# Kernel tuning notes

Measured on AMD Instinct MI355X. Metric: run time of the kernel, lower is better.

## Reference

```python
import jax, jax.numpy as jnp
import numpy as np

DEPTH_REF = jnp.array([28.01, 16.32], dtype=jnp.float32)
DIM_REF = jnp.array([[3.88, 1.63, 1.53], [0.84, 1.76, 0.66], [1.78, 1.52, 1.78]], dtype=jnp.float32)
TOPK = 50
DET_THRESHOLD = 0.25
PI = 3.14159265358979


def nms_hm(heat, kernel=3):
    # 3x3 max-pool NMS: keep peaks, zero everything else
    pad = (kernel - 1) // 2
    hmax = jax.lax.reduce_window(heat, -jnp.inf, jax.lax.max,
                                 (1, 1, kernel, kernel), (1, 1, 1, 1),
                                 [(0, 0), (0, 0), (pad, pad), (pad, pad)])
    return jnp.where(hmax == heat, heat, 0.0)


def select_topk(heat, K):
    B, C, H, W = heat.shape
    scores_all, inds_all = jax.lax.top_k(heat.reshape(B, C, H * W), K)  # [B,C,K]
    ys_all = (inds_all // W).astype(jnp.float32)
    xs_all = (inds_all % W).astype(jnp.float32)
    scores, inds = jax.lax.top_k(scores_all.reshape(B, C * K), K)       # [B,K] over classes
    clses = (inds // K).astype(jnp.float32)
    topk_inds = jnp.take_along_axis(inds_all.reshape(B, C * K), inds, axis=1)
    ys = jnp.take_along_axis(ys_all.reshape(B, C * K), inds, axis=1)
    xs = jnp.take_along_axis(xs_all.reshape(B, C * K), inds, axis=1)
    return scores, topk_inds, clses, ys, xs


def select_point_of_interest(index, feature_maps):
    B, Cf, H, W = feature_maps.shape
    fm = feature_maps.transpose(0, 2, 3, 1).reshape(B, H * W, Cf)
    return jnp.take_along_axis(fm, index[:, :, None], axis=1)  # [B,K,Cf]


def encode_box3d(rotys, dims, locs):
    # dims = (l, h, w); corner signs reproduce SMOKE's gather pattern
    N = rotys.shape[0]
    c, s = jnp.cos(rotys), jnp.sin(rotys)
    z, o = jnp.zeros_like(c), jnp.ones_like(c)
    ry = jnp.stack([c, z, s, z, o, z, -s, z, c], axis=1).reshape(N, 3, 3)
    sx = jnp.array([-0.5, 0.5, 0.5, 0.5, 0.5, -0.5, -0.5, -0.5], dtype=dims.dtype)
    sy = jnp.array([-1., -1., 0., 0., -1., -1., 0., 0.], dtype=dims.dtype)
    sz = jnp.array([-0.5, -0.5, -0.5, 0.5, 0.5, 0.5, 0.5, -0.5], dtype=dims.dtype)
    corners = jnp.stack([dims[:, 0:1] * sx, dims[:, 1:2] * sy, dims[:, 2:3] * sz], axis=1)  # [N,3,8]
    return jnp.einsum('nij,njk->nik', ry, corners) + locs[:, :, None]


def setup_inputs() -> dict:
    key = jax.random.key(0)
    k1, k2 = jax.random.split(key)
    B, C, H, W = 32, 3, 192, 640
    IMG_W, IMG_H = 4 * W, 4 * H
    pred_heatmap = jax.random.uniform(k1, (B, C, H, W), dtype=jnp.float32)
    pred_regression = jax.random.normal(k2, (B, 8, H, W), dtype=jnp.float32) * 0.5
    # affine image->heatmap (scale 1/4), invertible
    tm = jnp.array([[0.25, 0., 0.], [0., 0.25, 0.], [0., 0., 1.]], dtype=jnp.float32)
    trans_mat = jnp.tile(tm[None], (B, 1, 1))
    Kc = jnp.array([[721.5, 0., IMG_W / 2.], [0., 721.5, IMG_H / 2.], [0., 0., 1.]], dtype=jnp.float32)
    K_mat = jnp.tile(Kc[None], (B, 1, 1))
    img_size = jnp.tile(jnp.array([[IMG_W, IMG_H]], dtype=jnp.float32), (B, 1))
    return {"pred_heatmap": pred_heatmap, "pred_regression": pred_regression,
            "trans_mat": trans_mat, "K_mat": K_mat, "img_size": img_size}


def reference(pred_heatmap, pred_regression, trans_mat, K_mat, img_size):
    B = pred_heatmap.shape[0]
    heat = nms_hm(pred_heatmap)
    scores, inds, clses, ys, xs = select_topk(heat, TOPK)
    reg = select_point_of_interest(inds, pred_regression).reshape(-1, 8)  # [B*K,8]

    points = jnp.stack([xs.reshape(-1), ys.reshape(-1)], axis=1)          # heatmap coords
    depth_off, proj_off = reg[:, 0], reg[:, 1:3]
    dim_off, ori = reg[:, 3:6], reg[:, 6:8]
    cls_idx = clses.reshape(-1).astype(jnp.int32)

    obj_id = jnp.repeat(jnp.arange(B), TOPK)
    tm_inv = jnp.linalg.inv(trans_mat)[obj_id]   # [N,3,3]
    K_inv = jnp.linalg.inv(K_mat)[obj_id]

    # decode location: heatmap -> image -> camera frame
    proj = points + proj_off
    proj_ext = jnp.concatenate([proj, jnp.ones_like(proj[:, :1])], axis=1)
    proj_img = jnp.einsum('nij,nj->ni', tm_inv, proj_ext)                 # image-plane homog coords
    depths = depth_off * DEPTH_REF[1] + DEPTH_REF[0]
    locs = jnp.einsum('nij,nj->ni', K_inv, proj_img * depths[:, None])

    dims = jnp.exp(dim_off) * DIM_REF[cls_idx]                            # (l,h,w)
    locs = locs.at[:, 1].add(dims[:, 1] / 2)

    # decode orientation
    eps = 1e-7
    rays = jnp.arctan(locs[:, 0] / (locs[:, 2] + eps))
    alphas = jnp.arctan(ori[:, 0] / (ori[:, 1] + eps))
    alphas = jnp.where(ori[:, 1] >= 0, alphas - PI / 2, alphas + PI / 2)
    rotys = alphas + rays
    wrap = lambda a: jnp.where(a > PI, a - 2 * PI, jnp.where(a < -PI, a + 2 * PI, a))
    rotys, alphas = wrap(rotys), wrap(alphas)

    # encode 2D boxes from projected 3D corners
    corners = encode_box3d(rotys, dims, locs)                             # [N,3,8]
    proj2 = jnp.einsum('nij,njk->nik', K_mat[obj_id], corners)
    xy = proj2[:, :2] / proj2[:, 2:3]
    Wi, Hi = img_size[obj_id, 0], img_size[obj_id, 1]
    xmins = jnp.clip(xy[:, 0].min(axis=1), 0.0, Wi)
    ymins = jnp.clip(xy[:, 1].min(axis=1), 0.0, Hi)
    xmaxs = jnp.clip(xy[:, 0].max(axis=1), 0.0, Wi)
    ymaxs = jnp.clip(xy[:, 1].max(axis=1), 0.0, Hi)
    box2d = jnp.stack([xmins, ymins, xmaxs, ymaxs], axis=1)

    dims_rolled = jnp.roll(dims, -1, axis=1)                              # (h,w,l)
    result = jnp.concatenate([
        cls_idx.astype(jnp.float32)[:, None], alphas[:, None], box2d,
        dims_rolled, locs, rotys[:, None], scores.reshape(-1, 1)], axis=1)  # [B*K,14]
    keep = result[:, -1] > DET_THRESHOLD
    return jnp.where(keep[:, None], result, 0.0)
```

## Files before the change

### kernel.cpp

```cpp
#include <hip/hip_runtime.h>
#include <math.h>

#define Hd 192
#define Wd 640
#define HWp (Hd * Wd)
#define NCLS 3
#define KTOP 50
#define NB 32
#define NPL (NB * NCLS)
#define GPR 160
#define GPP (HWp / 4)
#define SPR 40
#define SPP (Hd * SPR)
#define SEGBLK 30
#define SEGCAP 64
#define CAP 2048
#define RBK 256
#define PI_F 3.14159265358979f

__device__ inline float fmax3(float a, float b, float c) {
  return fmaxf(fmaxf(a, b), c);
}

template <typename F>
__device__ inline void peaks_in_group(const float* __restrict__ p, int g, F&& f) {
  const int y = g / GPR;
  const int x0 = (g - y * GPR) * 4;
  const float* rm = p + y * Wd + x0;
  const float4 mq = *(const float4*)rm;
  const float ml = (x0 > 0) ? rm[-1] : -INFINITY;
  const float mr = (x0 + 4 < Wd) ? rm[4] : -INFINITY;
  float4 tq; float tl, tr;
  if (y > 0) {
    const float* rt = rm - Wd;
    tq = *(const float4*)rt;
    tl = (x0 > 0) ? rt[-1] : -INFINITY;
    tr = (x0 + 4 < Wd) ? rt[4] : -INFINITY;
  } else {
    tq.x = tq.y = tq.z = tq.w = -INFINITY; tl = -INFINITY; tr = -INFINITY;
  }
  float4 bq; float bl, br;
  if (y < Hd - 1) {
    const float* rb = rm + Wd;
    bq = *(const float4*)rb;
    bl = (x0 > 0) ? rb[-1] : -INFINITY;
    br = (x0 + 4 < Wd) ? rb[4] : -INFINITY;
  } else {
    bq.x = bq.y = bq.z = bq.w = -INFINITY; bl = -INFINITY; br = -INFINITY;
  }
  const float c0 = fmax3(tl, ml, bl);
  const float c1 = fmax3(tq.x, mq.x, bq.x);
  const float c2 = fmax3(tq.y, mq.y, bq.y);
  const float c3 = fmax3(tq.z, mq.z, bq.z);
  const float c4 = fmax3(tq.w, mq.w, bq.w);
  const float c5 = fmax3(tr, mr, br);
  const int base = y * Wd + x0;
  if (mq.x == fmax3(c0, c1, c2)) f(__float_as_uint(mq.x), base + 0);
  if (mq.y == fmax3(c1, c2, c3)) f(__float_as_uint(mq.y), base + 1);
  if (mq.z == fmax3(c2, c3, c4)) f(__float_as_uint(mq.z), base + 2);
  if (mq.w == fmax3(c3, c4, c5)) f(__float_as_uint(mq.w), base + 3);
}

template <typename F>
__device__ inline void for_each_peak_plane(const float* __restrict__ p, int tid,
                                           int nth, F&& f) {
  for (int g = tid; g < GPP; g += nth) peaks_in_group(p, g, f);
}

__device__ inline unsigned long long mk_key(unsigned int bits, int idx) {
  return ((unsigned long long)bits << 32) | (unsigned int)~idx;
}

__device__ inline int bucket_of(unsigned int bits) {
  const unsigned int base = __float_as_uint(0.995f);
  if (bits <= base) return 0;
  unsigned int d = (bits - base) >> 9;
  return d > 255u ? 255 : (int)d;
}

struct Row16 {
  float4 q0, q1, q2, q3;
  float l, r;
};

__device__ inline Row16 load_row16(const float* __restrict__ rp, int x0, bool valid) {
  Row16 o;
  if (valid) {
    o.q0 = *(const float4*)(rp);
    o.q1 = *(const float4*)(rp + 4);
    o.q2 = *(const float4*)(rp + 8);
    o.q3 = *(const float4*)(rp + 12);
    o.l = (x0 > 0) ? rp[-1] : -INFINITY;
    o.r = (x0 + 16 < Wd) ? rp[16] : -INFINITY;
  } else {
    o.q0.x = o.q0.y = o.q0.z = o.q0.w = -INFINITY;
    o.q1 = o.q0; o.q2 = o.q0; o.q3 = o.q0;
    o.l = -INFINITY; o.r = -INFINITY;
  }
  return o;
}

__device__ inline float4 max3v(const float4 a, const float4 b, const float4 c) {
  float4 o;
  o.x = fmax3(a.x, b.x, c.x);
  o.y = fmax3(a.y, b.y, c.y);
  o.z = fmax3(a.z, b.z, c.z);
  o.w = fmax3(a.w, b.w, c.w);
  return o;
}

__global__ __launch_bounds__(256) void scan_kernel(
    const float* __restrict__ heat,
    int* __restrict__ counts,
    unsigned long long* __restrict__ segkey) {
  const int blk = blockIdx.x;
  const int plane = blk / SEGBLK;
  const int sub = blk - plane * SEGBLK;
  __shared__ unsigned long long s_k[SEGCAP];
  __shared__ int s_n;
  if (threadIdx.x == 0) s_n = 0;
  __syncthreads();

  const int strip = sub * 256 + threadIdx.x;
  const int y = strip / SPR;
  const int x0 = (strip - y * SPR) * 16;
  const float* pm = heat + (size_t)plane * HWp + y * Wd + x0;

  const Row16 m = load_row16(pm, x0, true);
  const Row16 t = load_row16(pm - Wd, x0, y > 0);
  const Row16 b = load_row16(pm + Wd, x0, y < Hd - 1);

  const float cl = fmax3(t.l, m.l, b.l);
  const float cr = fmax3(t.r, m.r, b.r);
  const float4 c0 = max3v(t.q0, m.q0, b.q0);
  const float4 c1 = max3v(t.q1, m.q1, b.q1);
  const float4 c2 = max3v(t.q2, m.q2, b.q2);
  const float4 c3 = max3v(t.q3, m.q3, b.q3);

  const float TH = 0.995f;
  const int base = y * Wd + x0;
#define EMIT(V, W0, W1, W2, J)                                         \
  if ((V) >= TH && (V) == fmax3((W0), (W1), (W2))) {                   \
    int slot = atomicAdd(&s_n, 1);                                     \
    if (slot < SEGCAP) s_k[slot] = mk_key(__float_as_uint(V), base + (J)); \
  }
  EMIT(m.q0.x, cl,   c0.x, c0.y, 0)
  EMIT(m.q0.y, c0.x, c0.y, c0.z, 1)
  EMIT(m.q0.z, c0.y, c0.z, c0.w, 2)
  EMIT(m.q0.w, c0.z, c0.w, c1.x, 3)
  EMIT(m.q1.x, c0.w, c1.x, c1.y, 4)
  EMIT(m.q1.y, c1.x, c1.y, c1.z, 5)
  EMIT(m.q1.z, c1.y, c1.z, c1.w, 6)
  EMIT(m.q1.w, c1.z, c1.w, c2.x, 7)
  EMIT(m.q2.x, c1.w, c2.x, c2.y, 8)
  EMIT(m.q2.y, c2.x, c2.y, c2.z, 9)
  EMIT(m.q2.z, c2.y, c2.z, c2.w, 10)
  EMIT(m.q2.w, c2.z, c2.w, c3.x, 11)
  EMIT(m.q3.x, c2.w, c3.x, c3.y, 12)
  EMIT(m.q3.y, c3.x, c3.y, c3.z, 13)
  EMIT(m.q3.z, c3.y, c3.z, c3.w, 14)
  EMIT(m.q3.w, c3.z, c3.w, cr,   15)
#undef EMIT

  __syncthreads();
  const int n = s_n;
  if (threadIdx.x == 0) counts[blk] = n;
  const int nn = n < SEGCAP ? n : SEGCAP;
  if (threadIdx.x < nn)
    segkey[(size_t)blk * SEGCAP + threadIdx.x] = s_k[threadIdx.x];
}

__device__ inline void inv3(const float* m, float* o) {
  float a = m[0], b = m[1], c = m[2];
  float d = m[3], e = m[4], f = m[5];
  float g = m[6], h = m[7], i = m[8];
  float A = e * i - f * h;
  float B = -(d * i - f * g);
  float C = d * h - e * g;
  float det = a * A + b * B + c * C;
  float id = 1.0f / det;
  o[0] = A * id;            o[1] = -(b * i - c * h) * id; o[2] = (b * f - c * e) * id;
  o[3] = B * id;            o[4] = (a * i - c * g) * id;  o[5] = -(a * f - c * d) * id;
  o[6] = C * id;            o[7] = -(a * h - b * g) * id; o[8] = (a * e - b * d) * id;
}

__device__ inline float wrap_pi(float a) {
  if (a > PI_F) return a - 2.0f * PI_F;
  if (a < -PI_F) return a + 2.0f * PI_F;
  return a;
}

__constant__ float DIM_REF_C[9] = {3.88f, 1.63f, 1.53f,
                                   0.84f, 1.76f, 0.66f,
                                   1.78f, 1.52f, 1.78f};

__global__ __launch_bounds__(256) void rank_decode_kernel(
    const float* __restrict__ heat,
    const int* __restrict__ counts,
    const unsigned long long* __restrict__ segkey,
    const float* __restrict__ regr,
    const float* __restrict__ trans_mat,
    const float* __restrict__ K_mat,
    const float* __restrict__ img_size,
    float* __restrict__ out) {
  const int b = blockIdx.x;
  const int tid = threadIdx.x;

  __shared__ unsigned long long s_key[CAP];
  __shared__ unsigned long long g_key[CAP];
  __shared__ int s_off[SEGBLK + 1];
  __shared__ int cnt[RBK], suf[RBK], cur[RBK];
  __shared__ unsigned int fb_hist[1024];
  __shared__ float cls_sc[NCLS * KTOP];
  __shared__ int cls_pi[NCLS * KTOP];
  __shared__ int sel[KTOP];
  __shared__ int s_flag, s_cnt, s_B, s_above, s_T;

  for (int c = 0; c < NCLS; ++c) {
    const int plane = b * NCLS + c;
    __syncthreads();
    if (tid == 0) { s_flag = 0; s_off[0] = 0; }
    __syncthreads();
    if (tid < SEGBLK) {
      int n = counts[plane * SEGBLK + tid];
      if (n > SEGCAP) { atomicOr(&s_flag, 1); n = SEGCAP; }
      s_off[tid + 1] = n;
    }
    __syncthreads();
    if (tid == 0) {
      int acc = 0;
      for (int i = 1; i <= SEGBLK; ++i) { acc += s_off[i]; s_off[i] = acc; }
    }
    __syncthreads();
    int M = s_off[SEGBLK];
    const bool fast = (s_flag == 0) && (M >= KTOP) && (M <= CAP);

    if (fast) {
      const unsigned long long* pk = segkey + (size_t)plane * SEGBLK * SEGCAP;
      for (int i = tid; i < SEGBLK * SEGCAP; i += 256) {
        const int s = i >> 6;
        const int j = i & (SEGCAP - 1);
        const int o = s_off[s];
        const int n = s_off[s + 1] - o;
        if (j < n) s_key[o + j] = pk[(size_t)s * SEGCAP + j];
      }
      __syncthreads();
    } else {
      const float* p = heat + (size_t)plane * HWp;
      for (int i = tid; i < 1024; i += 256) fb_hist[i] = 0;
      __syncthreads();
      for_each_peak_plane(p, tid, 256, [&](unsigned int bits, int idx) {
        unsigned int bkt = bits >> 20; if (bkt > 1023u) bkt = 1023u;
        atomicAdd(&fb_hist[bkt], 1u);
      });
      __syncthreads();
      if (tid == 0) {
        int acc = 0, Bs = -1;
        for (int bkt = 1023; bkt >= 0; --bkt) {
          int cc = (int)fb_hist[bkt];
          if (acc + cc >= KTOP) { Bs = bkt; s_above = acc; break; }
          acc += cc;
        }
        s_B = Bs;
        if (Bs < 0) s_above = acc;
      }
      __syncthreads();
      const int Bs = s_B;
      unsigned int T;
      if (Bs < 0) {
        T = 0;
      } else {
        for (int i = tid; i < 1024; i += 256) fb_hist[i] = 0;
        __syncthreads();
        for_each_peak_plane(p, tid, 256, [&](unsigned int bits, int idx) {
          unsigned int bkt = bits >> 20; if (bkt > 1023u) bkt = 1023u;
          if ((int)bkt == Bs) atomicAdd(&fb_hist[(bits >> 10) & 1023], 1u);
        });
        __syncthreads();
        if (tid == 0) {
          int acc = s_above, Ss = 0;
          for (int sb = 1023; sb >= 0; --sb) {
            int cc = (int)fb_hist[sb];
            if (acc + cc >= KTOP) { Ss = sb; break; }
            acc += cc;
          }
          s_T = (int)(((unsigned int)Bs << 20) | ((unsigned int)Ss << 10));
        }
        __syncthreads();
        T = (unsigned int)s_T;
      }
      if (tid == 0) s_cnt = 0;
      __syncthreads();
      for_each_peak_plane(p, tid, 256, [&](unsigned int bits, int idx) {
        if (bits >= T) {
          int slot = atomicAdd(&s_cnt, 1);
          if (slot < CAP) s_key[slot] = mk_key(bits, idx);
        }
      });
      __syncthreads();
      M = s_cnt < CAP ? s_cnt : CAP;
    }

    for (int i = tid; i < RBK; i += 256) { cnt[i] = 0; cur[i] = 0; }
    __syncthreads();
    for (int i = tid; i < M; i += 256)
      atomicAdd(&cnt[bucket_of((unsigned int)(s_key[i] >> 32))], 1);
    __syncthreads();
    if (tid == 0) {
      int acc = 0;
      for (int bq = RBK - 1; bq >= 0; --bq) { suf[bq] = acc; acc += cnt[bq]; }
    }
    __syncthreads();
    for (int i = tid; i < M; i += 256) {
      const unsigned long long k = s_key[i];
      const int bq = bucket_of((unsigned int)(k >> 32));
      const int slot = suf[bq] + atomicAdd(&cur[bq], 1);
      g_key[slot] = k;
    }
    __syncthreads();
    for (int i = tid; i < M; i += 256) {
      const unsigned long long k = g_key[i];
      const int bq = bucket_of((unsigned int)(k >> 32));
      const int st = suf[bq];
      const int nb = cnt[bq];
      int rank = st;
      for (int t = st; t < st + nb; ++t) rank += (g_key[t] > k);
      if (rank < KTOP) {
        cls_sc[c * KTOP + rank] = __uint_as_float((unsigned int)(k >> 32));
        cls_pi[c * KTOP + rank] = (int)~((unsigned int)k);
      }
    }
    for (int s2 = M + tid; s2 < KTOP; s2 += 256) {
      cls_sc[c * KTOP + s2] = 0.0f;
      cls_pi[c * KTOP + s2] = 0;
    }
  }
  __syncthreads();

  if (tid < NCLS * KTOP) {
    const float v = cls_sc[tid];
    int rank = 0;
    for (int j = 0; j < NCLS * KTOP; ++j) {
      const float w = cls_sc[j];
      rank += (w > v) || (w == v && j < tid);
    }
    if (rank < KTOP) sel[rank] = tid;
  }
  __syncthreads();

  if (tid < KTOP) {
    const int i = sel[tid];
    const int cls = i / KTOP;
    const float score = cls_sc[i];
    const int ind = cls_pi[i];
    const float ys = (float)(ind / Wd);
    const float xs = (float)(ind - (ind / Wd) * Wd);

    const float* rb = regr + (size_t)b * 8 * HWp + ind;
    const float r0 = rb[0 * HWp], r1 = rb[1 * HWp], r2 = rb[2 * HWp], r3 = rb[3 * HWp];
    const float r4 = rb[4 * HWp], r5 = rb[5 * HWp], r6 = rb[6 * HWp], r7 = rb[7 * HWp];

    float tm[9], km[9], tmi[9], kmi[9];
#pragma unroll
    for (int q = 0; q < 9; ++q) { tm[q] = trans_mat[b * 9 + q]; km[q] = K_mat[b * 9 + q]; }
    inv3(tm, tmi);
    inv3(km, kmi);

    const float px = xs + r1, py = ys + r2;
    const float gx = tmi[0] * px + tmi[1] * py + tmi[2];
    const float gy = tmi[3] * px + tmi[4] * py + tmi[5];
    const float gz = tmi[6] * px + tmi[7] * py + tmi[8];
    const float depth = r0 * 16.32f + 28.01f;
    const float qx = gx * depth, qy = gy * depth, qz = gz * depth;
    const float lx = kmi[0] * qx + kmi[1] * qy + kmi[2] * qz;
    float ly = kmi[3] * qx + kmi[4] * qy + kmi[5] * qz;
    const float lz = kmi[6] * qx + kmi[7] * qy + kmi[8] * qz;

    const float d0 = expf(r3) * DIM_REF_C[cls * 3 + 0];
    const float d1 = expf(r4) * DIM_REF_C[cls * 3 + 1];
    const float d2 = expf(r5) * DIM_REF_C[cls * 3 + 2];
    ly += d1 * 0.5f;

    const float ray = atanf(lx / (lz + 1e-7f));
    float alpha = atanf(r6 / (r7 + 1e-7f));
    alpha += (r7 >= 0.0f) ? -PI_F * 0.5f : PI_F * 0.5f;
    const float roty = wrap_pi(alpha + ray);
    alpha = wrap_pi(alpha);

    const float SX[8] = {-0.5f, 0.5f, 0.5f, 0.5f, 0.5f, -0.5f, -0.5f, -0.5f};
    const float SY[8] = {-1.0f, -1.0f, 0.0f, 0.0f, -1.0f, -1.0f, 0.0f, 0.0f};
    const float SZ[8] = {-0.5f, -0.5f, -0.5f, 0.5f, 0.5f, 0.5f, 0.5f, -0.5f};
    const float cr = cosf(roty), sr = sinf(roty);
    float minx = INFINITY, maxx = -INFINITY, miny = INFINITY, maxy = -INFINITY;
#pragma unroll
    for (int j = 0; j < 8; ++j) {
      const float ax = d0 * SX[j], ay = d1 * SY[j], az = d2 * SZ[j];
      const float cx = cr * ax + sr * az + lx;
      const float cy = ay + ly;
      const float cz = -sr * ax + cr * az + lz;
      const float ppx = km[0] * cx + km[1] * cy + km[2] * cz;
      const float ppy = km[3] * cx + km[4] * cy + km[5] * cz;
      const float ppz = km[6] * cx + km[7] * cy + km[8] * cz;
      const float X = ppx / ppz, Y = ppy / ppz;
      minx = fminf(minx, X); maxx = fmaxf(maxx, X);
      miny = fminf(miny, Y); maxy = fmaxf(maxy, Y);
    }
    const float Wi = img_size[b * 2 + 0], Hi = img_size[b * 2 + 1];
    const float xmin = fminf(fmaxf(minx, 0.0f), Wi);
    const float ymin = fminf(fmaxf(miny, 0.0f), Hi);
    const float xmax = fminf(fmaxf(maxx, 0.0f), Wi);
    const float ymax = fminf(fmaxf(maxy, 0.0f), Hi);

    float* o = out + (size_t)(b * KTOP + tid) * 14;
    if (score > 0.25f) {
      o[0] = (float)cls; o[1] = alpha;
      o[2] = xmin; o[3] = ymin; o[4] = xmax; o[5] = ymax;
      o[6] = d1; o[7] = d2; o[8] = d0;
      o[9] = lx; o[10] = ly; o[11] = lz;
      o[12] = roty; o[13] = score;
    } else {
#pragma unroll
      for (int q = 0; q < 14; ++q) o[q] = 0.0f;
    }
  }
}


extern "C" void kernel_launch(void* const* d_in, const int* in_sizes, int n_in,
                              void* d_out, int out_size, void* d_ws, size_t ws_size,
                              hipStream_t stream) {
  const float* heat = (const float*)d_in[0];
  const float* regr = (const float*)d_in[1];
  const float* tmat = (const float*)d_in[2];
  const float* kmat = (const float*)d_in[3];
  const float* isz = (const float*)d_in[4];

  char* ws = (char*)d_ws;
  int* counts = (int*)ws;
  unsigned long long* segkey = (unsigned long long*)(ws + NPL * SEGBLK * 4);

  scan_kernel<<<NPL * SEGBLK, 256, 0, stream>>>(heat, counts, segkey);
  rank_decode_kernel<<<NB, 256, 0, stream>>>(heat, counts, segkey,
                                             regr, tmat, kmat, isz, (float*)d_out);
}
```

Measured before the change: 230.6 us.

## Split per-plane ranking into its own kernel with one block per plane

The per-batch rank+decode kernel looped serially over three class planes in a single block per batch. That work now lives in a separate kernel with one block per (batch, class) plane, which triples block parallelism and writes per-plane top-K to workspace. A third small kernel then merges across classes and decodes. This adds a kernel launch and a global round-trip for the intermediate scores and indices.

```diff
diff --git a/kernel.cpp b/kernel.cpp
--- a/kernel.cpp
+++ b/kernel.cpp
@@ -11,7 +11,6 @@
 #define GPR 160
 #define GPP (HWp / 4)
 #define SPR 40
-#define SPP (Hd * SPR)
 #define SEGBLK 30
 #define SEGCAP 64
 #define CAP 2048
@@ -170,6 +169,140 @@
     segkey[(size_t)blk * SEGCAP + threadIdx.x] = s_k[threadIdx.x];
 }
 
+__global__ __launch_bounds__(256) void plane_rank_kernel(
+    const float* __restrict__ heat,
+    const int* __restrict__ counts,
+    const unsigned long long* __restrict__ segkey,
+    float* __restrict__ out_scores,
+    int* __restrict__ out_inds) {
+  const int plane = blockIdx.x;
+  const int tid = threadIdx.x;
+
+  __shared__ unsigned long long s_key[CAP];
+  __shared__ unsigned long long g_key[CAP];
+  __shared__ int s_off[SEGBLK + 1];
+  __shared__ int cnt[RBK], suf[RBK], cur[RBK];
+  __shared__ unsigned int fb_hist[1024];
+  __shared__ int s_flag, s_cnt, s_B, s_above, s_T;
+
+  if (tid == 0) { s_flag = 0; s_off[0] = 0; }
+  __syncthreads();
+  if (tid < SEGBLK) {
+    int n = counts[plane * SEGBLK + tid];
+    if (n > SEGCAP) { atomicOr(&s_flag, 1); n = SEGCAP; }
+    s_off[tid + 1] = n;
+  }
+  __syncthreads();
+  if (tid == 0) {
+    int acc = 0;
+    for (int i = 1; i <= SEGBLK; ++i) { acc += s_off[i]; s_off[i] = acc; }
+  }
+  __syncthreads();
+  int M = s_off[SEGBLK];
+  const bool fast = (s_flag == 0) && (M >= KTOP) && (M <= CAP);
+
+  if (fast) {
+    const unsigned long long* pk = segkey + (size_t)plane * SEGBLK * SEGCAP;
+    for (int i = tid; i < SEGBLK * SEGCAP; i += 256) {
+      const int s = i >> 6;
+      const int j = i & (SEGCAP - 1);
+      const int o = s_off[s];
+      const int n = s_off[s + 1] - o;
+      if (j < n) s_key[o + j] = pk[(size_t)s * SEGCAP + j];
+    }
+    __syncthreads();
+  } else {
+    const float* p = heat + (size_t)plane * HWp;
+    for (int i = tid; i < 1024; i += 256) fb_hist[i] = 0;
+    __syncthreads();
+    for_each_peak_plane(p, tid, 256, [&](unsigned int bits, int idx) {
+      unsigned int bkt = bits >> 20; if (bkt > 1023u) bkt = 1023u;
+      atomicAdd(&fb_hist[bkt], 1u);
+    });
+    __syncthreads();
+    if (tid == 0) {
+      int acc = 0, Bs = -1;
+      for (int bkt = 1023; bkt >= 0; --bkt) {
+        int cc = (int)fb_hist[bkt];
+        if (acc + cc >= KTOP) { Bs = bkt; s_above = acc; break; }
+        acc += cc;
+      }
+      s_B = Bs;
+      if (Bs < 0) s_above = acc;
+    }
+    __syncthreads();
+    const int Bs = s_B;
+    unsigned int T;
+    if (Bs < 0) {
+      T = 0;
+    } else {
+      for (int i = tid; i < 1024; i += 256) fb_hist[i] = 0;
+      __syncthreads();
+      for_each_peak_plane(p, tid, 256, [&](unsigned int bits, int idx) {
+        unsigned int bkt = bits >> 20; if (bkt > 1023u) bkt = 1023u;
+        if ((int)bkt == Bs) atomicAdd(&fb_hist[(bits >> 10) & 1023], 1u);
+      });
+      __syncthreads();
+      if (tid == 0) {
+        int acc = s_above, Ss = 0;
+        for (int sb = 1023; sb >= 0; --sb) {
+          int cc = (int)fb_hist[sb];
+          if (acc + cc >= KTOP) { Ss = sb; break; }
+          acc += cc;
+        }
+        s_T = (int)(((unsigned int)Bs << 20) | ((unsigned int)Ss << 10));
+      }
+      __syncthreads();
+      T = (unsigned int)s_T;
+    }
+    if (tid == 0) s_cnt = 0;
+    __syncthreads();
+    for_each_peak_plane(p, tid, 256, [&](unsigned int bits, int idx) {
+      if (bits >= T) {
+        int slot = atomicAdd(&s_cnt, 1);
+        if (slot < CAP) s_key[slot] = mk_key(bits, idx);
+      }
+    });
+    __syncthreads();
+    M = s_cnt < CAP ? s_cnt : CAP;
+  }
+
+  for (int i = tid; i < RBK; i += 256) { cnt[i] = 0; cur[i] = 0; }
+  __syncthreads();
+  for (int i = tid; i < M; i += 256)
+    atomicAdd(&cnt[bucket_of((unsigned int)(s_key[i] >> 32))], 1);
+  __syncthreads();
+  if (tid == 0) {
+    int acc = 0;
+    for (int bq = RBK - 1; bq >= 0; --bq) { suf[bq] = acc; acc += cnt[bq]; }
+  }
+  __syncthreads();
+  for (int i = tid; i < M; i += 256) {
+    const unsigned long long k = s_key[i];
+    const int bq = bucket_of((unsigned int)(k >> 32));
+    const int slot = suf[bq] + atomicAdd(&cur[bq], 1);
+    g_key[slot] = k;
+  }
+  __syncthreads();
+  for (int i = tid; i < M; i += 256) {
+    const unsigned long long k = g_key[i];
+    const int bq = bucket_of((unsigned int)(k >> 32));
+    const int st = suf[bq];
+    const int nb = cnt[bq];
+    int rank = st;
+    for (int t = st; t < st + nb; ++t) rank += (g_key[t] > k);
+    if (rank < KTOP) {
+      out_scores[plane * KTOP + rank] = __uint_as_float((unsigned int)(k >> 32));
+      out_inds[plane * KTOP + rank] = (int)~((unsigned int)k);
+    }
+  }
+  __syncthreads();
+  for (int s2 = M + tid; s2 < KTOP; s2 += 256) {
+    out_scores[plane * KTOP + s2] = 0.0f;
+    out_inds[plane * KTOP + s2] = 0;
+  }
+}
+
 __device__ inline void inv3(const float* m, float* o) {
   float a = m[0], b = m[1], c = m[2];
   float d = m[3], e = m[4], f = m[5];
@@ -194,154 +327,31 @@
                                    0.84f, 1.76f, 0.66f,
                                    1.78f, 1.52f, 1.78f};
 
-__global__ __launch_bounds__(256) void rank_decode_kernel(
-    const float* __restrict__ heat,
-    const int* __restrict__ counts,
-    const unsigned long long* __restrict__ segkey,
+__global__ __launch_bounds__(192) void decode_kernel(
     const float* __restrict__ regr,
     const float* __restrict__ trans_mat,
     const float* __restrict__ K_mat,
     const float* __restrict__ img_size,
+    const float* __restrict__ ws_scores,
+    const int* __restrict__ ws_inds,
     float* __restrict__ out) {
   const int b = blockIdx.x;
   const int tid = threadIdx.x;
-
-  __shared__ unsigned long long s_key[CAP];
-  __shared__ unsigned long long g_key[CAP];
-  __shared__ int s_off[SEGBLK + 1];
-  __shared__ int cnt[RBK], suf[RBK], cur[RBK];
-  __shared__ unsigned int fb_hist[1024];
-  __shared__ float cls_sc[NCLS * KTOP];
-  __shared__ int cls_pi[NCLS * KTOP];
+  __shared__ float sc[NCLS * KTOP];
+  __shared__ int pi[NCLS * KTOP];
   __shared__ int sel[KTOP];
-  __shared__ int s_flag, s_cnt, s_B, s_above, s_T;
-
-  for (int c = 0; c < NCLS; ++c) {
-    const int plane = b * NCLS + c;
-    __syncthreads();
-    if (tid == 0) { s_flag = 0; s_off[0] = 0; }
-    __syncthreads();
-    if (tid < SEGBLK) {
-      int n = counts[plane * SEGBLK + tid];
-      if (n > SEGCAP) { atomicOr(&s_flag, 1); n = SEGCAP; }
-      s_off[tid + 1] = n;
-    }
-    __syncthreads();
-    if (tid == 0) {
-      int acc = 0;
-      for (int i = 1; i <= SEGBLK; ++i) { acc += s_off[i]; s_off[i] = acc; }
-    }
-    __syncthreads();
-    int M = s_off[SEGBLK];
-    const bool fast = (s_flag == 0) && (M >= KTOP) && (M <= CAP);
-
-    if (fast) {
-      const unsigned long long* pk = segkey + (size_t)plane * SEGBLK * SEGCAP;
-      for (int i = tid; i < SEGBLK * SEGCAP; i += 256) {
-        const int s = i >> 6;
-        const int j = i & (SEGCAP - 1);
-        const int o = s_off[s];
-        const int n = s_off[s + 1] - o;
-        if (j < n) s_key[o + j] = pk[(size_t)s * SEGCAP + j];
-      }
-      __syncthreads();
-    } else {
-      const float* p = heat + (size_t)plane * HWp;
-      for (int i = tid; i < 1024; i += 256) fb_hist[i] = 0;
-      __syncthreads();
-      for_each_peak_plane(p, tid, 256, [&](unsigned int bits, int idx) {
-        unsigned int bkt = bits >> 20; if (bkt > 1023u) bkt = 1023u;
-        atomicAdd(&fb_hist[bkt], 1u);
-      });
-      __syncthreads();
-      if (tid == 0) {
-        int acc = 0, Bs = -1;
-        for (int bkt = 1023; bkt >= 0; --bkt) {
-          int cc = (int)fb_hist[bkt];
-          if (acc + cc >= KTOP) { Bs = bkt; s_above = acc; break; }
-          acc += cc;
-        }
-        s_B = Bs;
-        if (Bs < 0) s_above = acc;
-      }
-      __syncthreads();
-      const int Bs = s_B;
-      unsigned int T;
-      if (Bs < 0) {
-        T = 0;
-      } else {
-        for (int i = tid; i < 1024; i += 256) fb_hist[i] = 0;
-        __syncthreads();
-        for_each_peak_plane(p, tid, 256, [&](unsigned int bits, int idx) {
-          unsigned int bkt = bits >> 20; if (bkt > 1023u) bkt = 1023u;
-          if ((int)bkt == Bs) atomicAdd(&fb_hist[(bits >> 10) & 1023], 1u);
-        });
-        __syncthreads();
-        if (tid == 0) {
-          int acc = s_above, Ss = 0;
-          for (int sb = 1023; sb >= 0; --sb) {
-            int cc = (int)fb_hist[sb];
-            if (acc + cc >= KTOP) { Ss = sb; break; }
-            acc += cc;
-          }
-          s_T = (int)(((unsigned int)Bs << 20) | ((unsigned int)Ss << 10));
-        }
-        __syncthreads();
-        T = (unsigned int)s_T;
-      }
-      if (tid == 0) s_cnt = 0;
-      __syncthreads();
-      for_each_peak_plane(p, tid, 256, [&](unsigned int bits, int idx) {
-        if (bits >= T) {
-          int slot = atomicAdd(&s_cnt, 1);
-          if (slot < CAP) s_key[slot] = mk_key(bits, idx);
-        }
-      });
-      __syncthreads();
-      M = s_cnt < CAP ? s_cnt : CAP;
-    }
-
-    for (int i = tid; i < RBK; i += 256) { cnt[i] = 0; cur[i] = 0; }
-    __syncthreads();
-    for (int i = tid; i < M; i += 256)
-      atomicAdd(&cnt[bucket_of((unsigned int)(s_key[i] >> 32))], 1);
-    __syncthreads();
-    if (tid == 0) {
-      int acc = 0;
-      for (int bq = RBK - 1; bq >= 0; --bq) { suf[bq] = acc; acc += cnt[bq]; }
-    }
-    __syncthreads();
-    for (int i = tid; i < M; i += 256) {
-      const unsigned long long k = s_key[i];
-      const int bq = bucket_of((unsigned int)(k >> 32));
-      const int slot = suf[bq] + atomicAdd(&cur[bq], 1);
-      g_key[slot] = k;
-    }
-    __syncthreads();
-    for (int i = tid; i < M; i += 256) {
-      const unsigned long long k = g_key[i];
-      const int bq = bucket_of((unsigned int)(k >> 32));
-      const int st = suf[bq];
-      const int nb = cnt[bq];
-      int rank = st;
-      for (int t = st; t < st + nb; ++t) rank += (g_key[t] > k);
-      if (rank < KTOP) {
-        cls_sc[c * KTOP + rank] = __uint_as_float((unsigned int)(k >> 32));
-        cls_pi[c * KTOP + rank] = (int)~((unsigned int)k);
-      }
-    }
-    for (int s2 = M + tid; s2 < KTOP; s2 += 256) {
-      cls_sc[c * KTOP + s2] = 0.0f;
-      cls_pi[c * KTOP + s2] = 0;
-    }
-  }
-  __syncthreads();
 
   if (tid < NCLS * KTOP) {
-    const float v = cls_sc[tid];
+    sc[tid] = ws_scores[b * NCLS * KTOP + tid];
+    pi[tid] = ws_inds[b * NCLS * KTOP + tid];
+  }
+  __syncthreads();
+
+  if (tid < NCLS * KTOP) {
+    const float v = sc[tid];
     int rank = 0;
     for (int j = 0; j < NCLS * KTOP; ++j) {
-      const float w = cls_sc[j];
+      const float w = sc[j];
       rank += (w > v) || (w == v && j < tid);
     }
     if (rank < KTOP) sel[rank] = tid;
@@ -351,8 +361,8 @@
   if (tid < KTOP) {
     const int i = sel[tid];
     const int cls = i / KTOP;
-    const float score = cls_sc[i];
-    const int ind = cls_pi[i];
+    const float score = sc[i];
+    const int ind = pi[i];
     const float ys = (float)(ind / Wd);
     const float xs = (float)(ind - (ind / Wd) * Wd);
 
@@ -437,9 +447,14 @@
 
   char* ws = (char*)d_ws;
   int* counts = (int*)ws;
-  unsigned long long* segkey = (unsigned long long*)(ws + NPL * SEGBLK * 4);
+  unsigned long long* segkey = (unsigned long long*)(ws + 16384);
+  char* after_seg = ws + 16384 + (size_t)NPL * SEGBLK * SEGCAP * 8;
+  float* ws_scores = (float*)after_seg;
+  int* ws_inds = (int*)(after_seg + NPL * KTOP * sizeof(float));
 
   scan_kernel<<<NPL * SEGBLK, 256, 0, stream>>>(heat, counts, segkey);
-  rank_decode_kernel<<<NB, 256, 0, stream>>>(heat, counts, segkey,
-                                             regr, tmat, kmat, isz, (float*)d_out);
-}
+  plane_rank_kernel<<<NPL, 256, 0, stream>>>(heat, counts, segkey,
+                                             ws_scores, ws_inds);
+  decode_kernel<<<NB, 192, 0, stream>>>(regr, tmat, kmat, isz,
+                                        ws_scores, ws_inds, (float*)d_out);
+}
```

New measurement: 212.5 us. 1.09x faster.

## Process all three class planes concurrently in one 768-thread rank block

Applied to the files above, without the earlier changes.

The rank/decode kernel now launches 768 threads per batch, and each 256-thread group handles one class plane at the same time instead of looping over classes one after another. Shared buffers are replicated per class. The heatmap fallback path is shared, with all 768 threads working on each non-fast plane in turn. This is meant to cut the serial per-class latency of this 32-block kernel, at the cost of roughly triple the shared memory (about 100KB) and one larger block per batch.

```diff
diff --git a/kernel.cpp b/kernel.cpp
--- a/kernel.cpp
+++ b/kernel.cpp
@@ -11,7 +11,6 @@
 #define GPR 160
 #define GPP (HWp / 4)
 #define SPR 40
-#define SPP (Hd * SPR)
 #define SEGBLK 30
 #define SEGCAP 64
 #define CAP 2048
@@ -194,7 +193,7 @@
                                    0.84f, 1.76f, 0.66f,
                                    1.78f, 1.52f, 1.78f};
 
-__global__ __launch_bounds__(256) void rank_decode_kernel(
+__global__ __launch_bounds__(768) void rank3_decode_kernel(
     const float* __restrict__ heat,
     const int* __restrict__ counts,
     const unsigned long long* __restrict__ segkey,
@@ -205,135 +204,156 @@
     float* __restrict__ out) {
   const int b = blockIdx.x;
   const int tid = threadIdx.x;
-
-  __shared__ unsigned long long s_key[CAP];
-  __shared__ unsigned long long g_key[CAP];
-  __shared__ int s_off[SEGBLK + 1];
-  __shared__ int cnt[RBK], suf[RBK], cur[RBK];
+  const int g = tid >> 8;
+  const int t = tid & 255;
+
+  __shared__ unsigned long long s_key[NCLS][CAP];
+  __shared__ unsigned long long g_key[NCLS][CAP];
+  __shared__ int s_off[NCLS][SEGBLK + 1];
+  __shared__ int cnt[NCLS][RBK], suf[NCLS][RBK], cur[NCLS][RBK];
   __shared__ unsigned int fb_hist[1024];
   __shared__ float cls_sc[NCLS * KTOP];
   __shared__ int cls_pi[NCLS * KTOP];
   __shared__ int sel[KTOP];
-  __shared__ int s_flag, s_cnt, s_B, s_above, s_T;
-
-  for (int c = 0; c < NCLS; ++c) {
-    const int plane = b * NCLS + c;
-    __syncthreads();
-    if (tid == 0) { s_flag = 0; s_off[0] = 0; }
-    __syncthreads();
-    if (tid < SEGBLK) {
-      int n = counts[plane * SEGBLK + tid];
-      if (n > SEGCAP) { atomicOr(&s_flag, 1); n = SEGCAP; }
-      s_off[tid + 1] = n;
-    }
-    __syncthreads();
-    if (tid == 0) {
-      int acc = 0;
-      for (int i = 1; i <= SEGBLK; ++i) { acc += s_off[i]; s_off[i] = acc; }
-    }
-    __syncthreads();
-    int M = s_off[SEGBLK];
-    const bool fast = (s_flag == 0) && (M >= KTOP) && (M <= CAP);
-
-    if (fast) {
-      const unsigned long long* pk = segkey + (size_t)plane * SEGBLK * SEGCAP;
-      for (int i = tid; i < SEGBLK * SEGCAP; i += 256) {
-        const int s = i >> 6;
-        const int j = i & (SEGCAP - 1);
-        const int o = s_off[s];
-        const int n = s_off[s + 1] - o;
-        if (j < n) s_key[o + j] = pk[(size_t)s * SEGCAP + j];
-      }
-      __syncthreads();
-    } else {
-      const float* p = heat + (size_t)plane * HWp;
-      for (int i = tid; i < 1024; i += 256) fb_hist[i] = 0;
-      __syncthreads();
-      for_each_peak_plane(p, tid, 256, [&](unsigned int bits, int idx) {
-        unsigned int bkt = bits >> 20; if (bkt > 1023u) bkt = 1023u;
-        atomicAdd(&fb_hist[bkt], 1u);
-      });
-      __syncthreads();
-      if (tid == 0) {
-        int acc = 0, Bs = -1;
-        for (int bkt = 1023; bkt >= 0; --bkt) {
-          int cc = (int)fb_hist[bkt];
-          if (acc + cc >= KTOP) { Bs = bkt; s_above = acc; break; }
-          acc += cc;
+  __shared__ int s_flag[NCLS], s_M[NCLS], s_fast[NCLS], s_all_fast;
+  __shared__ int fb_cnt, fb_B, fb_above, fb_T;
+
+  const int plane = b * NCLS + g;
+
+  if (tid == 0) s_all_fast = 1;
+  if (t == 0) { s_flag[g] = 0; s_off[g][0] = 0; }
+  __syncthreads();
+  if (t < SEGBLK) {
+    int n = counts[plane * SEGBLK + t];
+    if (n > SEGCAP) { atomicOr(&s_flag[g], 1); n = SEGCAP; }
+    s_off[g][t + 1] = n;
+  }
+  __syncthreads();
+  if (t == 0) {
+    int acc = 0;
+    for (int i = 1; i <= SEGBLK; ++i) { acc += s_off[g][i]; s_off[g][i] = acc; }
+    s_M[g] = acc;
+    const int fast = (s_flag[g] == 0) && (acc >= KTOP) && (acc <= CAP);
+    s_fast[g] = fast;
+    if (!fast) s_all_fast = 0;
+  }
+  __syncthreads();
+
+  if (s_all_fast) {
+    const unsigned long long* pk = segkey + (size_t)plane * SEGBLK * SEGCAP;
+    for (int i = t; i < SEGBLK * SEGCAP; i += 256) {
+      const int s = i >> 6;
+      const int j = i & (SEGCAP - 1);
+      const int o = s_off[g][s];
+      const int n = s_off[g][s + 1] - o;
+      if (j < n) s_key[g][o + j] = pk[(size_t)s * SEGCAP + j];
+    }
+  } else {
+    for (int p = 0; p < NCLS; ++p) {
+      if (s_fast[p]) {
+        const unsigned long long* pk =
+            segkey + (size_t)(b * NCLS + p) * SEGBLK * SEGCAP;
+        for (int i = tid; i < SEGBLK * SEGCAP; i += 768) {
+          const int s = i >> 6;
+          const int j = i & (SEGCAP - 1);
+          const int o = s_off[p][s];
+          const int n = s_off[p][s + 1] - o;
+          if (j < n) s_key[p][o + j] = pk[(size_t)s * SEGCAP + j];
         }
-        s_B = Bs;
-        if (Bs < 0) s_above = acc;
-      }
-      __syncthreads();
-      const int Bs = s_B;
-      unsigned int T;
-      if (Bs < 0) {
-        T = 0;
+        __syncthreads();
       } else {
-        for (int i = tid; i < 1024; i += 256) fb_hist[i] = 0;
-        __syncthreads();
-        for_each_peak_plane(p, tid, 256, [&](unsigned int bits, int idx) {
+        const float* hp = heat + (size_t)(b * NCLS + p) * HWp;
+        for (int i = tid; i < 1024; i += 768) fb_hist[i] = 0;
+        __syncthreads();
+        for_each_peak_plane(hp, tid, 768, [&](unsigned int bits, int idx) {
           unsigned int bkt = bits >> 20; if (bkt > 1023u) bkt = 1023u;
-          if ((int)bkt == Bs) atomicAdd(&fb_hist[(bits >> 10) & 1023], 1u);
+          atomicAdd(&fb_hist[bkt], 1u);
         });
         __syncthreads();
         if (tid == 0) {
-          int acc = s_above, Ss = 0;
-          for (int sb = 1023; sb >= 0; --sb) {
-            int cc = (int)fb_hist[sb];
-            if (acc + cc >= KTOP) { Ss = sb; break; }
+          int acc = 0, Bs = -1;
+          for (int bkt = 1023; bkt >= 0; --bkt) {
+            int cc = (int)fb_hist[bkt];
+            if (acc + cc >= KTOP) { Bs = bkt; fb_above = acc; break; }
             acc += cc;
           }
-          s_T = (int)(((unsigned int)Bs << 20) | ((unsigned int)Ss << 10));
+          fb_B = Bs;
+          if (Bs < 0) fb_above = acc;
         }
         __syncthreads();
-        T = (unsigned int)s_T;
+        const int Bs = fb_B;
+        unsigned int T;
+        if (Bs < 0) {
+          T = 0;
+        } else {
+          for (int i = tid; i < 1024; i += 768) fb_hist[i] = 0;
+          __syncthreads();
+          for_each_peak_plane(hp, tid, 768, [&](unsigned int bits, int idx) {
+            unsigned int bkt = bits >> 20; if (bkt > 1023u) bkt = 1023u;
+            if ((int)bkt == Bs) atomicAdd(&fb_hist[(bits >> 10) & 1023], 1u);
+          });
+          __syncthreads();
+          if (tid == 0) {
+            int acc = fb_above, Ss = 0;
+            for (int sb = 1023; sb >= 0; --sb) {
+              int cc = (int)fb_hist[sb];
+              if (acc + cc >= KTOP) { Ss = sb; break; }
+              acc += cc;
+            }
+            fb_T = (int)(((unsigned int)Bs << 20) | ((unsigned int)Ss << 10));
+          }
+          __syncthreads();
+          T = (unsigned int)fb_T;
+        }
+        if (tid == 0) fb_cnt = 0;
+        __syncthreads();
+        for_each_peak_plane(hp, tid, 768, [&](unsigned int bits, int idx) {
+          if (bits >= T) {
+            int slot = atomicAdd(&fb_cnt, 1);
+            if (slot < CAP) s_key[p][slot] = mk_key(bits, idx);
+          }
+        });
+        __syncthreads();
+        if (tid == 0) s_M[p] = fb_cnt < CAP ? fb_cnt : CAP;
+        __syncthreads();
       }
-      if (tid == 0) s_cnt = 0;
-      __syncthreads();
-      for_each_peak_plane(p, tid, 256, [&](unsigned int bits, int idx) {
-        if (bits >= T) {
-          int slot = atomicAdd(&s_cnt, 1);
-          if (slot < CAP) s_key[slot] = mk_key(bits, idx);
-        }
-      });
-      __syncthreads();
-      M = s_cnt < CAP ? s_cnt : CAP;
-    }
-
-    for (int i = tid; i < RBK; i += 256) { cnt[i] = 0; cur[i] = 0; }
-    __syncthreads();
-    for (int i = tid; i < M; i += 256)
-      atomicAdd(&cnt[bucket_of((unsigned int)(s_key[i] >> 32))], 1);
-    __syncthreads();
-    if (tid == 0) {
-      int acc = 0;
-      for (int bq = RBK - 1; bq >= 0; --bq) { suf[bq] = acc; acc += cnt[bq]; }
-    }
-    __syncthreads();
-    for (int i = tid; i < M; i += 256) {
-      const unsigned long long k = s_key[i];
-      const int bq = bucket_of((unsigned int)(k >> 32));
-      const int slot = suf[bq] + atomicAdd(&cur[bq], 1);
-      g_key[slot] = k;
-    }
-    __syncthreads();
-    for (int i = tid; i < M; i += 256) {
-      const unsigned long long k = g_key[i];
-      const int bq = bucket_of((unsigned int)(k >> 32));
-      const int st = suf[bq];
-      const int nb = cnt[bq];
-      int rank = st;
-      for (int t = st; t < st + nb; ++t) rank += (g_key[t] > k);
-      if (rank < KTOP) {
-        cls_sc[c * KTOP + rank] = __uint_as_float((unsigned int)(k >> 32));
-        cls_pi[c * KTOP + rank] = (int)~((unsigned int)k);
-      }
-    }
-    for (int s2 = M + tid; s2 < KTOP; s2 += 256) {
-      cls_sc[c * KTOP + s2] = 0.0f;
-      cls_pi[c * KTOP + s2] = 0;
-    }
+    }
+  }
+  __syncthreads();
+  const int M = s_M[g];
+
+  for (int i = t; i < RBK; i += 256) { cnt[g][i] = 0; cur[g][i] = 0; }
+  __syncthreads();
+  for (int i = t; i < M; i += 256)
+    atomicAdd(&cnt[g][bucket_of((unsigned int)(s_key[g][i] >> 32))], 1);
+  __syncthreads();
+  if (t == 0) {
+    int acc = 0;
+    for (int bq = RBK - 1; bq >= 0; --bq) { suf[g][bq] = acc; acc += cnt[g][bq]; }
+  }
+  __syncthreads();
+  for (int i = t; i < M; i += 256) {
+    const unsigned long long k = s_key[g][i];
+    const int bq = bucket_of((unsigned int)(k >> 32));
+    const int slot = suf[g][bq] + atomicAdd(&cur[g][bq], 1);
+    g_key[g][slot] = k;
+  }
+  __syncthreads();
+  for (int i = t; i < M; i += 256) {
+    const unsigned long long k = g_key[g][i];
+    const int bq = bucket_of((unsigned int)(k >> 32));
+    const int st = suf[g][bq];
+    const int nb = cnt[g][bq];
+    int rank = st;
+    for (int tt = st; tt < st + nb; ++tt) rank += (g_key[g][tt] > k);
+    if (rank < KTOP) {
+      cls_sc[g * KTOP + rank] = __uint_as_float((unsigned int)(k >> 32));
+      cls_pi[g * KTOP + rank] = (int)~((unsigned int)k);
+    }
+  }
+  for (int s2 = M + t; s2 < KTOP; s2 += 256) {
+    cls_sc[g * KTOP + s2] = 0.0f;
+    cls_pi[g * KTOP + s2] = 0;
   }
   __syncthreads();
 
@@ -437,9 +457,10 @@
 
   char* ws = (char*)d_ws;
   int* counts = (int*)ws;
-  unsigned long long* segkey = (unsigned long long*)(ws + NPL * SEGBLK * 4);
+  unsigned long long* segkey = (unsigned long long*)(ws + 16384);
 
   scan_kernel<<<NPL * SEGBLK, 256, 0, stream>>>(heat, counts, segkey);
-  rank_decode_kernel<<<NB, 256, 0, stream>>>(heat, counts, segkey,
-                                             regr, tmat, kmat, isz, (float*)d_out);
-}
+  rank3_decode_kernel<<<NB, 768, 0, stream>>>(heat, counts, segkey,
+                                              regr, tmat, kmat, isz,
+                                              (float*)d_out);
+}
```

Measured after the change: 211.4 us. 8.3% less time.
